# Optimization experiments

Measured on AMD Instinct MI355X. Metric: run time of the kernel, lower is better.

## Reference

```python
import jax, jax.numpy as jnp
import numpy as np

B, N, F, W = 8, 2048, 128, 64


def setup_inputs() -> dict:
    key = jax.random.key(0)
    k1, k2, k3, k4 = jax.random.split(key, 4)
    x = jax.random.normal(k1, (B, N, F), dtype=jnp.float32)
    adj = jnp.ones((B, N, N), dtype=bool)  # accepted by forward but unused
    w_key = jax.random.normal(k2, (F, W), dtype=jnp.float32) * 0.1
    w_value = jax.random.normal(k3, (F, F), dtype=jnp.float32) * 0.1
    w_query = jax.random.normal(k4, (F, W), dtype=jnp.float32) * 0.1
    return {"x": x, "adj": adj, "w_key": w_key, "w_value": w_value, "w_query": w_query}


def reference(x, adj, w_key, w_value, w_query):
    # keys/queries: [B, N, W]; values: [B, N, F]
    keys = x @ w_key
    querys = x @ w_query
    values = x @ w_value
    # per-batch softmax(Q K^T) over last dim -> [B, N, N]
    scores = jax.nn.softmax(jnp.einsum('bnw,bmw->bnm', querys, keys), axis=-1)
    # original broadcast-multiply-sum is exactly scores @ values
    out = jnp.einsum('bnm,bmf->bnf', scores, values)
    return out
```

## Files before the change

kernel.cpp:

```cpp
#include <hip/hip_runtime.h>
#include <hip/hip_bf16.h>
#include <math.h>

constexpr int B = 8;
constexpr int N = 2048;
constexpr int F = 128;
constexpr int W = 64;

constexpr int TQ = 128;
constexpr int TK = 64;
constexpr int KSPLIT = 4;
constexpr int TILES_PER_SPLIT = (N / TK) / KSPLIT;

typedef short bf16x8 __attribute__((ext_vector_type(8)));
typedef float f32x4  __attribute__((ext_vector_type(4)));

__device__ inline ushort f2bf(float f) {
  union { float f; uint u; } v; v.f = f;
  uint u = v.u;
  return (ushort)((u + 0x7FFFu + ((u >> 16) & 1u)) >> 16);
}
__device__ inline float bf2f(ushort h) {
  union { uint u; float f; } v; v.u = ((uint)h) << 16;
  return v.f;
}
__device__ inline void splitbf(float f, ushort& hi, ushort& lo) {
  ushort h = f2bf(f);
  hi = h;
  lo = f2bf(f - bf2f(h));
}

__global__ __launch_bounds__(256) void prep_w(
    const float* __restrict__ wq, const float* __restrict__ wk,
    const float* __restrict__ wv, ushort* __restrict__ wth,
    ushort* __restrict__ wtl) {
  int gid = blockIdx.x * 256 + threadIdx.x;
  int n = gid >> 4;
  int k0 = (gid & 15) * 8;
  ushort th[8], tl[8];
#pragma unroll
  for (int j = 0; j < 8; ++j) {
    int k = k0 + j;
    float val = (n < 64)  ? wq[k * W + n]
              : (n < 128) ? wk[k * W + (n - 64)]
                          : wv[k * F + (n - 128)];
    splitbf(val, th[j], tl[j]);
  }
  *(uint4*)&wth[n * 128 + k0] = *(uint4*)th;
  *(uint4*)&wtl[n * 128 + k0] = *(uint4*)tl;
}

__global__ __launch_bounds__(256) void proj_kernel(
    const float* __restrict__ x,
    const ushort* __restrict__ wth, const ushort* __restrict__ wtl,
    ushort* __restrict__ q_h, ushort* __restrict__ q_l,
    ushort* __restrict__ k_h, ushort* __restrict__ k_l,
    ushort* __restrict__ vt_ws) {
  const int tid  = threadIdx.x;
  const int wid  = tid >> 6;
  const int lane = tid & 63;
  const int lg = lane >> 4, li = lane & 15;
  const int rb   = blockIdx.x & 255;
  const int half = blockIdx.x >> 8;
  const int brow0 = rb * 64;
  const int b    = brow0 / N;
  const int nloc = brow0 % N;

  bf16x8 xh[4], xl[4];
  const float* xrow = x + (size_t)(brow0 + wid * 16 + li) * F;
#pragma unroll
  for (int kk = 0; kk < 4; ++kk) {
    float4 a = *(const float4*)&xrow[kk * 32 + lg * 8];
    float4 c = *(const float4*)&xrow[kk * 32 + lg * 8 + 4];
    float vals[8] = {a.x, a.y, a.z, a.w, c.x, c.y, c.z, c.w};
    ushort hh[8], ll[8];
#pragma unroll
    for (int j = 0; j < 8; ++j) splitbf(vals[j], hh[j], ll[j]);
    xh[kk] = *(bf16x8*)hh;
    xl[kk] = *(bf16x8*)ll;
  }

  f32x4 zero = {0.f, 0.f, 0.f, 0.f};
  f32x4 acc[8];
#pragma unroll
  for (int t = 0; t < 8; ++t) acc[t] = zero;

  const ushort* wbh = wth + (size_t)half * 128 * 128;
  const ushort* wbl = wtl + (size_t)half * 128 * 128;

  if (half == 0) {
#pragma unroll
    for (int kk = 0; kk < 4; ++kk)
#pragma unroll
      for (int nt = 0; nt < 8; ++nt) {
        bf16x8 bh = *(const bf16x8*)&wbh[(nt * 16 + li) * 128 + kk * 32 + lg * 8];
        bf16x8 bl = *(const bf16x8*)&wbl[(nt * 16 + li) * 128 + kk * 32 + lg * 8];
        acc[nt] = __builtin_amdgcn_mfma_f32_16x16x32_bf16(xh[kk], bh, acc[nt], 0, 0, 0);
        acc[nt] = __builtin_amdgcn_mfma_f32_16x16x32_bf16(xh[kk], bl, acc[nt], 0, 0, 0);
        acc[nt] = __builtin_amdgcn_mfma_f32_16x16x32_bf16(xl[kk], bh, acc[nt], 0, 0, 0);
      }
#pragma unroll
    for (int nt = 0; nt < 8; ++nt)
#pragma unroll
      for (int r = 0; r < 4; ++r) {
        int row = brow0 + wid * 16 + lg * 4 + r;
        int c = nt * 16 + li;
        ushort hv, lv;
        splitbf(acc[nt][r], hv, lv);
        if (nt < 4) { q_h[row * W + c] = hv;        q_l[row * W + c] = lv; }
        else        { k_h[row * W + (c - 64)] = hv; k_l[row * W + (c - 64)] = lv; }
      }
  } else {
#pragma unroll
    for (int kk = 0; kk < 4; ++kk)
#pragma unroll
      for (int mt = 0; mt < 8; ++mt) {
        bf16x8 ah = *(const bf16x8*)&wbh[(mt * 16 + li) * 128 + kk * 32 + lg * 8];
        bf16x8 al = *(const bf16x8*)&wbl[(mt * 16 + li) * 128 + kk * 32 + lg * 8];
        acc[mt] = __builtin_amdgcn_mfma_f32_16x16x32_bf16(ah, xh[kk], acc[mt], 0, 0, 0);
        acc[mt] = __builtin_amdgcn_mfma_f32_16x16x32_bf16(ah, xl[kk], acc[mt], 0, 0, 0);
        acc[mt] = __builtin_amdgcn_mfma_f32_16x16x32_bf16(al, xh[kk], acc[mt], 0, 0, 0);
      }
#pragma unroll
    for (int mt = 0; mt < 8; ++mt)
#pragma unroll
      for (int r = 0; r < 4; ++r) {
        int f = mt * 16 + lg * 4 + r;
        int n = nloc + wid * 16 + li;
        vt_ws[(size_t)b * F * N + (size_t)f * N + n] = f2bf(acc[mt][r]);
      }
  }
}

constexpr int LP = 72;

__global__ __launch_bounds__(512) void attn_kernel(
    const ushort* __restrict__ q_h, const ushort* __restrict__ q_l,
    const ushort* __restrict__ k_h, const ushort* __restrict__ k_l,
    const ushort* __restrict__ vt_ws,
    float* __restrict__ out,
    float* __restrict__ op1,
    float* __restrict__ op2,
    float* __restrict__ op3,
    float* __restrict__ lsums) {
  __shared__ ushort ksh[TK][LP];
  __shared__ ushort ksl[TK][LP];
  __shared__ ushort vst[F][LP];
  __shared__ ushort ps[8][16][LP];

  const int tid  = threadIdx.x;
  const int wid  = tid >> 6;
  const int lane = tid & 63;
  const int lg = lane >> 4, li = lane & 15;
  const int b = blockIdx.y, qt = blockIdx.x, split = blockIdx.z;

  const size_t koffb = (size_t)b * N * W;
  const ushort* vb = vt_ws + (size_t)b * F * N;

  const size_t qrow = (size_t)(b * N + qt * TQ + wid * 16 + li) * W;
  bf16x8 qah[2], qal[2];
  qah[0] = *(const bf16x8*)&q_h[qrow + lg * 8];
  qah[1] = *(const bf16x8*)&q_h[qrow + 32 + lg * 8];
  qal[0] = *(const bf16x8*)&q_l[qrow + lg * 8];
  qal[1] = *(const bf16x8*)&q_l[qrow + 32 + lg * 8];

  float l_lane = 0.f;
  f32x4 zero = {0.f, 0.f, 0.f, 0.f};
  f32x4 o_acc[8];
#pragma unroll
  for (int t = 0; t < 8; ++t) o_acc[t] = zero;

  const int kt0 = split * TILES_PER_SPLIT;
  for (int kt = kt0; kt < kt0 + TILES_PER_SPLIT; ++kt) {
    __syncthreads();
    const size_t koff = koffb + (size_t)kt * TK * W;
    {
      int row = tid >> 3, c8 = tid & 7;
      *(uint4*)&ksh[row][c8 * 8] = *(const uint4*)&k_h[koff + row * W + c8 * 8];
      *(uint4*)&ksl[row][c8 * 8] = *(const uint4*)&k_l[koff + row * W + c8 * 8];
    }
#pragma unroll
    for (int j = 0; j < 2; ++j) {
      int idx = tid + j * 512, f = idx >> 3, c8 = idx & 7;
      *(uint4*)&vst[f][c8 * 8] = *(const uint4*)&vb[(size_t)f * N + kt * TK + c8 * 8];
    }
    __syncthreads();

    f32x4 s_acc[4];
#pragma unroll
    for (int nt = 0; nt < 4; ++nt) s_acc[nt] = zero;
#pragma unroll
    for (int kk = 0; kk < 2; ++kk)
#pragma unroll
      for (int nt = 0; nt < 4; ++nt) {
        bf16x8 kh = *(const bf16x8*)&ksh[nt * 16 + li][kk * 32 + lg * 8];
        bf16x8 kl = *(const bf16x8*)&ksl[nt * 16 + li][kk * 32 + lg * 8];
        s_acc[nt] = __builtin_amdgcn_mfma_f32_16x16x32_bf16(kh, qah[kk], s_acc[nt], 0, 0, 0);
        s_acc[nt] = __builtin_amdgcn_mfma_f32_16x16x32_bf16(kh, qal[kk], s_acc[nt], 0, 0, 0);
        s_acc[nt] = __builtin_amdgcn_mfma_f32_16x16x32_bf16(kl, qah[kk], s_acc[nt], 0, 0, 0);
      }

#pragma unroll
    for (int nt = 0; nt < 4; ++nt)
#pragma unroll
      for (int r = 0; r < 4; ++r) {
        float p = __expf(s_acc[nt][r]);
        ushort ph = f2bf(p);
        l_lane += bf2f(ph);
        ps[wid][li][nt * 16 + lg * 4 + r] = ph;
      }

#pragma unroll
    for (int kk = 0; kk < 2; ++kk) {
      bf16x8 pa = *(const bf16x8*)&ps[wid][li][kk * 32 + lg * 8];
#pragma unroll
      for (int ft = 0; ft < 8; ++ft) {
        bf16x8 vf = *(const bf16x8*)&vst[ft * 16 + li][kk * 32 + lg * 8];
        o_acc[ft] = __builtin_amdgcn_mfma_f32_16x16x32_bf16(pa, vf, o_acc[ft], 0, 0, 0);
      }
    }
  }

  l_lane += __shfl_xor(l_lane, 16, 64);
  l_lane += __shfl_xor(l_lane, 32, 64);

  float* opb = (split == 0) ? out : (split == 1) ? op1 : (split == 2) ? op2 : op3;
  float* ob = opb + (size_t)(b * N + qt * TQ) * F;
#pragma unroll
  for (int r = 0; r < 4; ++r) {
    int row = wid * 16 + lg * 4 + r;
#pragma unroll
    for (int ft = 0; ft < 8; ++ft)
      ob[row * F + ft * 16 + li] = o_acc[ft][r];
  }
  if (lg == 0) {
    size_t gr = (size_t)split * B * N + (size_t)(b * N + qt * TQ) + wid * 16 + li;
    lsums[gr] = l_lane;
  }
}

__global__ __launch_bounds__(256) void combine_kernel(
    const float* __restrict__ op1, const float* __restrict__ op2,
    const float* __restrict__ op3, const float* __restrict__ lsums,
    float* __restrict__ out) {
  const int gr  = blockIdx.x * 2 + (threadIdx.x >> 7);
  const int col = threadIdx.x & 127;
  constexpr size_t BN = (size_t)B * N;
  const float l = lsums[gr] + lsums[BN + gr] + lsums[2 * BN + gr] + lsums[3 * BN + gr];
  const float inv = 1.f / l;
  const size_t idx = (size_t)gr * F + col;
  out[idx] = (out[idx] + op1[idx] + op2[idx] + op3[idx]) * inv;
}

extern "C" void kernel_launch(void* const* d_in, const int* in_sizes, int n_in,
                              void* d_out, int out_size, void* d_ws, size_t ws_size,
                              hipStream_t stream) {
  const float* x  = (const float*)d_in[0];
  const float* wk = (const float*)d_in[2];
  const float* wv = (const float*)d_in[3];
  const float* wq = (const float*)d_in[4];
  float* out = (float*)d_out;

  constexpr size_t BNW = (size_t)B * N * W;
  constexpr size_t BNF = (size_t)B * N * F;
  ushort* q_h  = (ushort*)d_ws;
  ushort* q_l  = q_h + BNW;
  ushort* k_h  = q_l + BNW;
  ushort* k_l  = k_h + BNW;
  ushort* vt   = k_l + BNW;
  ushort* wth  = vt + BNF;
  ushort* wtl  = wth + 32768;
  float*  op1  = (float*)(wtl + 32768);
  float*  op2  = op1 + BNF;
  float*  op3  = op2 + BNF;
  float*  ls   = op3 + BNF;

  prep_w<<<16, 256, 0, stream>>>(wq, wk, wv, wth, wtl);
  proj_kernel<<<512, 256, 0, stream>>>(x, wth, wtl, q_h, q_l, k_h, k_l, vt);
  dim3 grid(N / TQ, B, KSPLIT);
  attn_kernel<<<grid, 512, 0, stream>>>(q_h, q_l, k_h, k_l, vt,
                                        out, op1, op2, op3, ls);
  combine_kernel<<<B * N / 2, 256, 0, stream>>>(op1, op2, op3, ls, out);
}
```

Measured before the change: 235.1 us.

## Combine split-K attention partials with atomics and restructure projection blocks via LDS

The attention kernel now accumulates its four split-K partial outputs and row sums straight into the zeroed output and lsum buffers with float atomics. This removes the three extra partial-output buffers and the combine kernel's re-read of them, and adds two memsets and a lighter normalize pass. The projection kernel now gives each block 32 rows: the x tile is staged through shared memory once, and its warps split into a Q/K pass and a V pass, so x is split into hi/lo bf16 once per block instead of twice. Atomic accumulation makes the summation order nondeterministic and may contend on the output.

Result: slower. 252.9 us (+7.6%).

```diff
diff --git a/kernel.cpp b/kernel.cpp
--- a/kernel.cpp
+++ b/kernel.cpp
@@ -50,34 +50,43 @@
   *(uint4*)&wtl[n * 128 + k0] = *(uint4*)tl;
 }
 
+constexpr int KP = 136;
+
 __global__ __launch_bounds__(256) void proj_kernel(
     const float* __restrict__ x,
     const ushort* __restrict__ wth, const ushort* __restrict__ wtl,
     ushort* __restrict__ q_h, ushort* __restrict__ q_l,
     ushort* __restrict__ k_h, ushort* __restrict__ k_l,
     ushort* __restrict__ vt_ws) {
+  __shared__ ushort xsh[32][KP];
+  __shared__ ushort xsl[32][KP];
+
   const int tid  = threadIdx.x;
   const int wid  = tid >> 6;
   const int lane = tid & 63;
   const int lg = lane >> 4, li = lane & 15;
-  const int rb   = blockIdx.x & 255;
-  const int half = blockIdx.x >> 8;
-  const int brow0 = rb * 64;
+  const int pass = wid >> 1;
+  const int rg   = wid & 1;
+  const int brow0 = blockIdx.x * 32;
   const int b    = brow0 / N;
   const int nloc = brow0 % N;
 
+  for (int idx = tid; idx < 32 * 128 / 4; idx += 256) {
+    int row = idx >> 5, c4 = idx & 31;
+    float4 xv = *(const float4*)&x[(size_t)(brow0 + row) * F + c4 * 4];
+    ushort4 h, l;
+    splitbf(xv.x, h.x, l.x); splitbf(xv.y, h.y, l.y);
+    splitbf(xv.z, h.z, l.z); splitbf(xv.w, h.w, l.w);
+    *(ushort4*)&xsh[row][c4 * 4] = h;
+    *(ushort4*)&xsl[row][c4 * 4] = l;
+  }
+  __syncthreads();
+
   bf16x8 xh[4], xl[4];
-  const float* xrow = x + (size_t)(brow0 + wid * 16 + li) * F;
 #pragma unroll
   for (int kk = 0; kk < 4; ++kk) {
-    float4 a = *(const float4*)&xrow[kk * 32 + lg * 8];
-    float4 c = *(const float4*)&xrow[kk * 32 + lg * 8 + 4];
-    float vals[8] = {a.x, a.y, a.z, a.w, c.x, c.y, c.z, c.w};
-    ushort hh[8], ll[8];
-#pragma unroll
-    for (int j = 0; j < 8; ++j) splitbf(vals[j], hh[j], ll[j]);
-    xh[kk] = *(bf16x8*)hh;
-    xl[kk] = *(bf16x8*)ll;
+    xh[kk] = *(const bf16x8*)&xsh[rg * 16 + li][kk * 32 + lg * 8];
+    xl[kk] = *(const bf16x8*)&xsl[rg * 16 + li][kk * 32 + lg * 8];
   }
 
   f32x4 zero = {0.f, 0.f, 0.f, 0.f};
@@ -85,10 +94,10 @@
 #pragma unroll
   for (int t = 0; t < 8; ++t) acc[t] = zero;
 
-  const ushort* wbh = wth + (size_t)half * 128 * 128;
-  const ushort* wbl = wtl + (size_t)half * 128 * 128;
-
-  if (half == 0) {
+  const ushort* wbh = wth + (size_t)pass * 128 * 128;
+  const ushort* wbl = wtl + (size_t)pass * 128 * 128;
+
+  if (pass == 0) {
 #pragma unroll
     for (int kk = 0; kk < 4; ++kk)
 #pragma unroll
@@ -103,7 +112,7 @@
     for (int nt = 0; nt < 8; ++nt)
 #pragma unroll
       for (int r = 0; r < 4; ++r) {
-        int row = brow0 + wid * 16 + lg * 4 + r;
+        int row = brow0 + rg * 16 + lg * 4 + r;
         int c = nt * 16 + li;
         ushort hv, lv;
         splitbf(acc[nt][r], hv, lv);
@@ -126,7 +135,7 @@
 #pragma unroll
       for (int r = 0; r < 4; ++r) {
         int f = mt * 16 + lg * 4 + r;
-        int n = nloc + wid * 16 + li;
+        int n = nloc + rg * 16 + li;
         vt_ws[(size_t)b * F * N + (size_t)f * N + n] = f2bf(acc[mt][r]);
       }
   }
@@ -139,9 +148,6 @@
     const ushort* __restrict__ k_h, const ushort* __restrict__ k_l,
     const ushort* __restrict__ vt_ws,
     float* __restrict__ out,
-    float* __restrict__ op1,
-    float* __restrict__ op2,
-    float* __restrict__ op3,
     float* __restrict__ lsums) {
   __shared__ ushort ksh[TK][LP];
   __shared__ ushort ksl[TK][LP];
@@ -224,32 +230,28 @@
   l_lane += __shfl_xor(l_lane, 16, 64);
   l_lane += __shfl_xor(l_lane, 32, 64);
 
-  float* opb = (split == 0) ? out : (split == 1) ? op1 : (split == 2) ? op2 : op3;
-  float* ob = opb + (size_t)(b * N + qt * TQ) * F;
+  float* ob = out + (size_t)(b * N + qt * TQ) * F;
 #pragma unroll
   for (int r = 0; r < 4; ++r) {
     int row = wid * 16 + lg * 4 + r;
 #pragma unroll
     for (int ft = 0; ft < 8; ++ft)
-      ob[row * F + ft * 16 + li] = o_acc[ft][r];
-  }
-  if (lg == 0) {
-    size_t gr = (size_t)split * B * N + (size_t)(b * N + qt * TQ) + wid * 16 + li;
-    lsums[gr] = l_lane;
-  }
-}
-
-__global__ __launch_bounds__(256) void combine_kernel(
-    const float* __restrict__ op1, const float* __restrict__ op2,
-    const float* __restrict__ op3, const float* __restrict__ lsums,
-    float* __restrict__ out) {
-  const int gr  = blockIdx.x * 2 + (threadIdx.x >> 7);
-  const int col = threadIdx.x & 127;
-  constexpr size_t BN = (size_t)B * N;
-  const float l = lsums[gr] + lsums[BN + gr] + lsums[2 * BN + gr] + lsums[3 * BN + gr];
-  const float inv = 1.f / l;
-  const size_t idx = (size_t)gr * F + col;
-  out[idx] = (out[idx] + op1[idx] + op2[idx] + op3[idx]) * inv;
+      unsafeAtomicAdd(&ob[row * F + ft * 16 + li], o_acc[ft][r]);
+  }
+  if (lg == 0)
+    unsafeAtomicAdd(&lsums[(size_t)(b * N + qt * TQ) + wid * 16 + li], l_lane);
+}
+
+__global__ __launch_bounds__(256) void normalize_kernel(
+    const float* __restrict__ lsums, float* __restrict__ out) {
+  const int gid = blockIdx.x * 256 + threadIdx.x;
+  const int row = gid >> 5;
+  const int c4  = (gid & 31) * 4;
+  const float inv = 1.f / lsums[row];
+  float4* p = (float4*)&out[(size_t)row * F + c4];
+  float4 v = *p;
+  v.x *= inv; v.y *= inv; v.z *= inv; v.w *= inv;
+  *p = v;
 }
 
 extern "C" void kernel_launch(void* const* d_in, const int* in_sizes, int n_in,
@@ -270,15 +272,14 @@
   ushort* vt   = k_l + BNW;
   ushort* wth  = vt + BNF;
   ushort* wtl  = wth + 32768;
-  float*  op1  = (float*)(wtl + 32768);
-  float*  op2  = op1 + BNF;
-  float*  op3  = op2 + BNF;
-  float*  ls   = op3 + BNF;
+  float*  ls   = (float*)(wtl + 32768);
 
   prep_w<<<16, 256, 0, stream>>>(wq, wk, wv, wth, wtl);
-  proj_kernel<<<512, 256, 0, stream>>>(x, wth, wtl, q_h, q_l, k_h, k_l, vt);
+  proj_kernel<<<(B * N) / 32, 256, 0, stream>>>(x, wth, wtl,
+                                                q_h, q_l, k_h, k_l, vt);
+  hipMemsetAsync(out, 0, BNF * sizeof(float), stream);
+  hipMemsetAsync(ls, 0, (size_t)B * N * sizeof(float), stream);
   dim3 grid(N / TQ, B, KSPLIT);
-  attn_kernel<<<grid, 512, 0, stream>>>(q_h, q_l, k_h, k_l, vt,
-                                        out, op1, op2, op3, ls);
-  combine_kernel<<<B * N / 2, 256, 0, stream>>>(op1, op2, op3, ls, out);
-}
+  attn_kernel<<<grid, 512, 0, stream>>>(q_h, q_l, k_h, k_l, vt, out, ls);
+  normalize_kernel<<<(int)(BNF / 4 / 256), 256, 0, stream>>>(ls, out);
+}
```
